# Optimization experiments

Hardware: AMD Instinct MI355X
Metric: run time of the kernel (lower is better)

The kernel has to match this reference:

```python
import jax, jax.numpy as jnp
import numpy as np

EPS = 1e-5

def setup_inputs() -> dict:
    key = jax.random.key(0)
    k1, k2 = jax.random.split(key)
    x = jax.random.normal(k1, (64, 128, 56, 56), dtype=jnp.float32)
    weight = jax.random.normal(k2, (128, 128, 3, 3), dtype=jnp.float32)  # OIHW
    gamma = jnp.ones((128,), dtype=jnp.float32)   # bn.weight initialized to 1.0
    beta = jnp.zeros((128,), dtype=jnp.float32)   # bn.bias
    return {"x": x, "weight": weight, "gamma": gamma, "beta": beta}

def reference(x, weight, gamma, beta):
    # BinActive / eval-mode sign binarization of activations
    xb = jnp.sign(x)
    # BinaryConv2dKernel: conv with sign-binarized (+/-1) weights, stride 1, pad 1, no bias
    wb = jnp.sign(weight)
    y = jax.lax.conv_general_dilated(
        xb, wb,
        window_strides=(1, 1),
        padding=((1, 1), (1, 1)),
        dimension_numbers=("NCHW", "OIHW", "NCHW"),
    )
    # BatchNorm2d with batch statistics (biased variance), affine gamma/beta
    mean = jnp.mean(y, axis=(0, 2, 3), keepdims=True)           # [1,C,1,1]
    var = jnp.mean((y - mean) ** 2, axis=(0, 2, 3), keepdims=True)
    y_hat = (y - mean) * jax.lax.rsqrt(var + EPS)
    return y_hat * gamma[None, :, None, None] + beta[None, :, None, None]
```

## Files before the change

### kernel.cpp

```cpp
#include <hip/hip_runtime.h>
#include <stdint.h>

#define HH 56
#define WW 56
#define CC 128
#define OO 128
#define NIMG 64
#define PIX (HH*WW)
#define CNT (NIMG*PIX)
#define TOT ((size_t)NIMG*OO*PIX)

#define WS_WPACK 0
#define WS_STATS 18432
#define WS_SS    20480
#define WS_XPACK 32768
#define WS_Y16   3244032
#define WS_NEED  (3244032 + (size_t)TOT*2)

__global__ void pack_w_kernel(const float* __restrict__ w, ulonglong2* __restrict__ wpack) {
    int t = blockIdx.x * 256 + threadIdx.x;
    if (t >= OO * 9) return;
    int o = t / 9, tap = t % 9;
    const float* wp = w + (size_t)o * CC * 9 + tap;
    unsigned long long lo = 0, hi = 0;
    #pragma unroll 4
    for (int c = 0; c < 64; ++c) lo |= (unsigned long long)(wp[c * 9] > 0.0f) << c;
    #pragma unroll 4
    for (int c = 0; c < 64; ++c) hi |= (unsigned long long)(wp[(c + 64) * 9] > 0.0f) << c;
    wpack[t] = make_ulonglong2(lo, hi);
}

__global__ void pack_x_kernel(const float* __restrict__ x, ulonglong2* __restrict__ xpack) {
    int n = blockIdx.y;
    int p = blockIdx.x * 256 + threadIdx.x;
    if (p >= PIX) return;
    const float* xp = x + (size_t)n * CC * PIX + p;
    unsigned long long lo = 0, hi = 0;
    #pragma unroll 8
    for (int c = 0; c < 64; ++c) lo |= (unsigned long long)(xp[(size_t)c * PIX] > 0.0f) << c;
    #pragma unroll 8
    for (int c = 0; c < 64; ++c) hi |= (unsigned long long)(xp[(size_t)(c + 64) * PIX] > 0.0f) << c;
    xpack[n * PIX + p] = make_ulonglong2(lo, hi);
}

template <int MODE>
__global__ __launch_bounds__(256, 2) void conv_kernel(
    const ulonglong2* __restrict__ xpack,
    const ulonglong2* __restrict__ wpack,
    unsigned long long* stats,
    const float2* __restrict__ ss,
    short* __restrict__ y16,
    float* __restrict__ out)
{
    const int og = blockIdx.x;
    const int strip = blockIdx.y;
    const int n = blockIdx.z;
    const int tid = threadIdx.x;
    const int o_idx = tid & 31;
    const int wseg = tid >> 5;
    const int o = og * 32 + o_idx;
    const int w0 = wseg * 7;
    const int h0 = strip * 14;

    ulonglong2 wt[9];
    #pragma unroll
    for (int t = 0; t < 9; ++t) wt[t] = wpack[o * 9 + t];

    int f[9];
    #pragma unroll
    for (int t = 0; t < 9; ++t) f[t] = 128 - 2 * (__popcll(wt[t].x) + __popcll(wt[t].y));
    const int cr0 = f[0] + f[1] + f[2];
    const int cr2 = f[6] + f[7] + f[8];
    const int cc0 = f[0] + f[3] + f[6];
    const int cc2 = f[2] + f[5] + f[8];

    float scale = 0.f, shift = 0.f;
    if (MODE == 2) { float2 v = ss[o]; scale = v.x; shift = v.y; }

    const ulonglong2* xp = xpack + n * PIX;

    ulonglong2 rA[9], rB[9], rC[9];
    auto loadRow = [&](ulonglong2* R, int r) {
        if (r < 0 || r >= HH) {
            #pragma unroll
            for (int i = 0; i < 9; ++i) R[i] = make_ulonglong2(0ULL, 0ULL);
        } else {
            #pragma unroll
            for (int i = 0; i < 9; ++i) {
                int wp = w0 - 1 + i;
                R[i] = (wp >= 0 && wp < WW) ? xp[r * WW + wp] : make_ulonglong2(0ULL, 0ULL);
            }
        }
    };

    loadRow(rA, h0 - 1);
    loadRow(rB, h0);

    int ysum = 0, ysq = 0;

    for (int h = h0; h < h0 + 14; ++h) {
        loadRow(rC, h + 1);
        #pragma unroll
        for (int j = 0; j < 7; ++j) {
            int mis = 0;
            #pragma unroll
            for (int kw = 0; kw < 3; ++kw) {
                ulonglong2 a = rA[j + kw];
                mis += __popcll(a.x ^ wt[kw].x) + __popcll(a.y ^ wt[kw].y);
                ulonglong2 b = rB[j + kw];
                mis += __popcll(b.x ^ wt[3 + kw].x) + __popcll(b.y ^ wt[3 + kw].y);
                ulonglong2 c = rC[j + kw];
                mis += __popcll(c.x ^ wt[6 + kw].x) + __popcll(c.y ^ wt[6 + kw].y);
            }
            int y = 1152 - 2 * mis;
            int corr = 0;
            if (h == 0) corr += cr0;
            if (h == HH - 1) corr += cr2;
            if (j == 0 && wseg == 0) {
                corr += cc0;
                if (h == 0) corr -= f[0];
                if (h == HH - 1) corr -= f[6];
            }
            if (j == 6 && wseg == 7) {
                corr += cc2;
                if (h == 0) corr -= f[2];
                if (h == HH - 1) corr -= f[8];
            }
            y -= corr;
            if (MODE != 2) { ysum += y; ysq += y * y; }
            size_t oidx = ((size_t)(n * OO + o) * HH + h) * WW + (w0 + j);
            if (MODE == 1) y16[oidx] = (short)y;
            if (MODE == 2) out[oidx] = (float)y * scale + shift;
        }
        #pragma unroll
        for (int i = 0; i < 9; ++i) { rA[i] = rB[i]; rB[i] = rC[i]; }
    }

    if (MODE != 2) {
        __shared__ int s_sum[256];
        __shared__ int s_sq[256];
        s_sum[tid] = ysum;
        s_sq[tid] = ysq;
        __syncthreads();
        if (tid < 32) {
            long long ts = 0, tq = 0;
            #pragma unroll
            for (int k = 0; k < 8; ++k) { ts += s_sum[tid + 32 * k]; tq += s_sq[tid + 32 * k]; }
            int oo = og * 32 + tid;
            atomicAdd(&stats[oo * 2 + 0], (unsigned long long)ts);
            atomicAdd(&stats[oo * 2 + 1], (unsigned long long)tq);
        }
    }
}

__global__ void finalize_kernel(const unsigned long long* __restrict__ stats,
                                const float* __restrict__ gamma,
                                const float* __restrict__ beta,
                                float2* __restrict__ ss) {
    int c = threadIdx.x;
    if (c >= 128) return;
    long long s = (long long)stats[c * 2 + 0];
    long long q = (long long)stats[c * 2 + 1];
    double mean = (double)s / (double)CNT;
    double var = (double)q / (double)CNT - mean * mean;
    double inv = 1.0 / sqrt(var + 1e-5);
    double g = (double)gamma[c];
    float sc = (float)(g * inv);
    float sh = (float)((double)beta[c] - mean * g * inv);
    ss[c] = make_float2(sc, sh);
}

__global__ void norm_kernel(const short* __restrict__ y16,
                            const float2* __restrict__ ss,
                            float* __restrict__ out) {
    size_t g = (size_t)blockIdx.x * 256 + threadIdx.x;
    size_t e = g * 8;
    unsigned int chan = (unsigned int)((e / PIX) & 127);
    float2 v = ss[chan];
    int4 raw = *reinterpret_cast<const int4*>(y16 + e);
    float4 o0, o1;
    o0.x = (float)(short)(raw.x & 0xffff) * v.x + v.y;
    o0.y = (float)(short)(raw.x >> 16)    * v.x + v.y;
    o0.z = (float)(short)(raw.y & 0xffff) * v.x + v.y;
    o0.w = (float)(short)(raw.y >> 16)    * v.x + v.y;
    o1.x = (float)(short)(raw.z & 0xffff) * v.x + v.y;
    o1.y = (float)(short)(raw.z >> 16)    * v.x + v.y;
    o1.z = (float)(short)(raw.w & 0xffff) * v.x + v.y;
    o1.w = (float)(short)(raw.w >> 16)    * v.x + v.y;
    *reinterpret_cast<float4*>(out + e) = o0;
    *reinterpret_cast<float4*>(out + e + 4) = o1;
}

extern "C" void kernel_launch(void* const* d_in, const int* in_sizes, int n_in,
                              void* d_out, int out_size, void* d_ws, size_t ws_size,
                              hipStream_t stream) {
    const float* x     = (const float*)d_in[0];
    const float* wgt   = (const float*)d_in[1];
    const float* gamma = (const float*)d_in[2];
    const float* beta  = (const float*)d_in[3];
    float* out = (float*)d_out;
    char* ws = (char*)d_ws;

    ulonglong2* wpack = (ulonglong2*)(ws + WS_WPACK);
    unsigned long long* stats = (unsigned long long*)(ws + WS_STATS);
    float2* ss = (float2*)(ws + WS_SS);
    ulonglong2* xpack = (ulonglong2*)(ws + WS_XPACK);
    short* y16 = (short*)(ws + WS_Y16);

    hipMemsetAsync(stats, 0, 2048, stream);
    pack_w_kernel<<<5, 256, 0, stream>>>(wgt, wpack);
    pack_x_kernel<<<dim3(13, 64), 256, 0, stream>>>(x, xpack);

    if (ws_size >= WS_NEED) {
        conv_kernel<1><<<dim3(4, 4, 64), 256, 0, stream>>>(xpack, wpack, stats, nullptr, y16, nullptr);
        finalize_kernel<<<1, 128, 0, stream>>>(stats, gamma, beta, ss);
        norm_kernel<<<(unsigned)(TOT / 8 / 256), 256, 0, stream>>>(y16, ss, out);
    } else {
        conv_kernel<0><<<dim3(4, 4, 64), 256, 0, stream>>>(xpack, wpack, stats, nullptr, nullptr, nullptr);
        finalize_kernel<<<1, 128, 0, stream>>>(stats, gamma, beta, ss);
        conv_kernel<2><<<dim3(4, 4, 64), 256, 0, stream>>>(xpack, wpack, stats, ss, nullptr, out);
    }
}
```

Baseline: 156.7 us.

## Stage packed input tile in LDS and halve row strips per conv block

The conv kernel now loads a 9x58 halo tile of bit-packed input pixels into shared memory once per block, instead of having each thread read its 3x9 window from global memory row by row. Strip height drops from 14 to 7 rows, so the grid doubles, and launch bounds ask for 4 blocks per CU. Edge corrections are hoisted per row and a rotating 3-column register window is read from LDS. This cuts redundant global loads and register pressure, at the cost of an extra barrier, more halo rows relative to output rows, and possible LDS bank conflicts on 16-byte reads.

```diff
diff --git a/kernel.cpp b/kernel.cpp
--- a/kernel.cpp
+++ b/kernel.cpp
@@ -1,5 +1,6 @@
 #include <hip/hip_runtime.h>
 #include <stdint.h>
+
 
 #define HH 56
 #define WW 56
@@ -44,7 +45,7 @@
 }
 
 template <int MODE>
-__global__ __launch_bounds__(256, 2) void conv_kernel(
+__global__ __launch_bounds__(256, 4) void conv_kernel(
     const ulonglong2* __restrict__ xpack,
     const ulonglong2* __restrict__ wpack,
     unsigned long long* stats,
@@ -52,6 +53,10 @@
     short* __restrict__ y16,
     float* __restrict__ out)
 {
+    __shared__ ulonglong2 tile[9][58];
+    __shared__ int s_sum[256];
+    __shared__ int s_sq[256];
+
     const int og = blockIdx.x;
     const int strip = blockIdx.y;
     const int n = blockIdx.z;
@@ -60,7 +65,18 @@
     const int wseg = tid >> 5;
     const int o = og * 32 + o_idx;
     const int w0 = wseg * 7;
-    const int h0 = strip * 14;
+    const int h0 = strip * 7;
+
+    {
+        const ulonglong2* xp = xpack + n * PIX;
+        for (int i = tid; i < 9 * 58; i += 256) {
+            int r = i / 58, c = i % 58;
+            int gr = h0 - 1 + r, gc = c - 1;
+            ulonglong2 v = make_ulonglong2(0ULL, 0ULL);
+            if (gr >= 0 && gr < HH && gc >= 0 && gc < WW) v = xp[gr * WW + gc];
+            tile[r][c] = v;
+        }
+    }
 
     ulonglong2 wt[9];
     #pragma unroll
@@ -77,68 +93,55 @@
     float scale = 0.f, shift = 0.f;
     if (MODE == 2) { float2 v = ss[o]; scale = v.x; shift = v.y; }
 
-    const ulonglong2* xp = xpack + n * PIX;
-
-    ulonglong2 rA[9], rB[9], rC[9];
-    auto loadRow = [&](ulonglong2* R, int r) {
-        if (r < 0 || r >= HH) {
-            #pragma unroll
-            for (int i = 0; i < 9; ++i) R[i] = make_ulonglong2(0ULL, 0ULL);
-        } else {
-            #pragma unroll
-            for (int i = 0; i < 9; ++i) {
-                int wp = w0 - 1 + i;
-                R[i] = (wp >= 0 && wp < WW) ? xp[r * WW + wp] : make_ulonglong2(0ULL, 0ULL);
-            }
-        }
-    };
-
-    loadRow(rA, h0 - 1);
-    loadRow(rB, h0);
+    __syncthreads();
 
     int ysum = 0, ysq = 0;
 
-    for (int h = h0; h < h0 + 14; ++h) {
-        loadRow(rC, h + 1);
+    for (int hh = 0; hh < 7; ++hh) {
+        const int h = h0 + hh;
+        int base = 1152;
+        if (h == 0) base -= cr0;
+        if (h == HH - 1) base -= cr2;
+        int eL = (wseg == 0) ? (cc0 - ((h == 0) ? f[0] : 0) - ((h == HH - 1) ? f[6] : 0)) : 0;
+        int eR = (wseg == 7) ? (cc2 - ((h == 0) ? f[2] : 0) - ((h == HH - 1) ? f[8] : 0)) : 0;
+
+        const ulonglong2* trow = &tile[hh][w0];
+
+        ulonglong2 X[3][3];
+        #pragma unroll
+        for (int r = 0; r < 3; ++r) {
+            X[0][r] = trow[r * 58 + 0];
+            X[1][r] = trow[r * 58 + 1];
+        }
+
+        size_t obase = ((size_t)(n * OO + o) * HH + h) * WW + w0;
+
         #pragma unroll
         for (int j = 0; j < 7; ++j) {
-            int mis = 0;
             #pragma unroll
-            for (int kw = 0; kw < 3; ++kw) {
-                ulonglong2 a = rA[j + kw];
-                mis += __popcll(a.x ^ wt[kw].x) + __popcll(a.y ^ wt[kw].y);
-                ulonglong2 b = rB[j + kw];
-                mis += __popcll(b.x ^ wt[3 + kw].x) + __popcll(b.y ^ wt[3 + kw].y);
-                ulonglong2 c = rC[j + kw];
-                mis += __popcll(c.x ^ wt[6 + kw].x) + __popcll(c.y ^ wt[6 + kw].y);
+            for (int r = 0; r < 3; ++r) X[(j + 2) % 3][r] = trow[r * 58 + j + 2];
+
+            int m0 = 0, m1 = 0, m2 = 0;
+            #pragma unroll
+            for (int k = 0; k < 3; ++k) {
+                ulonglong2 a = X[(j + k) % 3][0];
+                m0 += __popcll(a.x ^ wt[k].x) + __popcll(a.y ^ wt[k].y);
+                ulonglong2 b = X[(j + k) % 3][1];
+                m1 += __popcll(b.x ^ wt[3 + k].x) + __popcll(b.y ^ wt[3 + k].y);
+                ulonglong2 c = X[(j + k) % 3][2];
+                m2 += __popcll(c.x ^ wt[6 + k].x) + __popcll(c.y ^ wt[6 + k].y);
             }
-            int y = 1152 - 2 * mis;
-            int corr = 0;
-            if (h == 0) corr += cr0;
-            if (h == HH - 1) corr += cr2;
-            if (j == 0 && wseg == 0) {
-                corr += cc0;
-                if (h == 0) corr -= f[0];
-                if (h == HH - 1) corr -= f[6];
-            }
-            if (j == 6 && wseg == 7) {
-                corr += cc2;
-                if (h == 0) corr -= f[2];
-                if (h == HH - 1) corr -= f[8];
-            }
-            y -= corr;
+            int y = base - 2 * (m0 + m1 + m2);
+            if (j == 0) y -= eL;
+            if (j == 6) y -= eR;
+
             if (MODE != 2) { ysum += y; ysq += y * y; }
-            size_t oidx = ((size_t)(n * OO + o) * HH + h) * WW + (w0 + j);
-            if (MODE == 1) y16[oidx] = (short)y;
-            if (MODE == 2) out[oidx] = (float)y * scale + shift;
-        }
-        #pragma unroll
-        for (int i = 0; i < 9; ++i) { rA[i] = rB[i]; rB[i] = rC[i]; }
+            if (MODE == 1) y16[obase + j] = (short)y;
+            if (MODE == 2) out[obase + j] = (float)y * scale + shift;
+        }
     }
 
     if (MODE != 2) {
-        __shared__ int s_sum[256];
-        __shared__ int s_sq[256];
         s_sum[tid] = ysum;
         s_sq[tid] = ysq;
         __syncthreads();
@@ -212,12 +215,12 @@
     pack_x_kernel<<<dim3(13, 64), 256, 0, stream>>>(x, xpack);
 
     if (ws_size >= WS_NEED) {
-        conv_kernel<1><<<dim3(4, 4, 64), 256, 0, stream>>>(xpack, wpack, stats, nullptr, y16, nullptr);
+        conv_kernel<1><<<dim3(4, 8, 64), 256, 0, stream>>>(xpack, wpack, stats, nullptr, y16, nullptr);
         finalize_kernel<<<1, 128, 0, stream>>>(stats, gamma, beta, ss);
         norm_kernel<<<(unsigned)(TOT / 8 / 256), 256, 0, stream>>>(y16, ss, out);
     } else {
-        conv_kernel<0><<<dim3(4, 4, 64), 256, 0, stream>>>(xpack, wpack, stats, nullptr, nullptr, nullptr);
+        conv_kernel<0><<<dim3(4, 8, 64), 256, 0, stream>>>(xpack, wpack, stats, nullptr, nullptr, nullptr);
         finalize_kernel<<<1, 128, 0, stream>>>(stats, gamma, beta, ss);
-        conv_kernel<2><<<dim3(4, 4, 64), 256, 0, stream>>>(xpack, wpack, stats, ss, nullptr, out);
-    }
-}
+        conv_kernel<2><<<dim3(4, 8, 64), 256, 0, stream>>>(xpack, wpack, stats, ss, nullptr, out);
+    }
+}
```

Result: slower. 243.3 us (+55.2%).
